# Kernel optimization log

Hardware: AMD Instinct MI355X
Metric: run time of the kernel (lower is better)

## Reference

```python
import jax, jax.numpy as jnp
import numpy as np

K = 16  # neighborhood size


def _eigen_ratio(pts, k):
    """pts: [B, N, 3] -> ratio lambda_max / lambda_mid per point, [B, N]."""
    pts = pts[..., :3]
    # pairwise squared distances [B, N, N]
    sq = jnp.sum(pts * pts, axis=-1)  # [B, N]
    d2 = sq[:, :, None] + sq[:, None, :] - 2.0 * jnp.einsum('bnd,bmd->bnm', pts, pts)
    # k nearest neighbors (self included, as in KNN(x, x))
    _, idx = jax.lax.top_k(-d2, k)  # idx: [B, N, k] int32
    # gather neighbor coordinates: [B, N, k, 3]
    neighbors = jax.vmap(lambda p, i: p[i])(pts, idx)
    mean = jnp.mean(neighbors, axis=2, keepdims=True)
    diff = neighbors - mean  # [B, N, k, 3]
    # covariance = mean over k of outer products -> [B, N, 3, 3]
    cov = jnp.einsum('bnki,bnkj->bnij', diff, diff) / k
    ev = jnp.linalg.eigvalsh(cov)  # ascending: [..., 3]
    return ev[..., 2] / ev[..., 1]


def setup_inputs() -> dict:
    key = jax.random.key(0)
    kx, ky = jax.random.split(key)
    x = jax.random.normal(kx, (2, 8192, 3), dtype=jnp.float32)
    y = jax.random.normal(ky, (2, 8192, 3), dtype=jnp.float32)
    return {"x": x, "y": y}


def reference(x, y):
    er1 = _eigen_ratio(x, K)  # [B, N]
    er2 = _eigen_ratio(y, K)
    res = jnp.mean((er1 - er2) ** 2, axis=-1)  # mean over points
    return jnp.mean(res)  # reduction='mean' over batch
```

## Files before the change

kernel.cpp:

```cpp
#include <hip/hip_runtime.h>
#include <hip/hip_bf16.h>
#include <math.h>

#define NPTS   8192
#define KNN    16
#define G      16
#define NCELL  (G * G * G)
#define NCHUNK 128
#define NPART  4

__constant__ float c_B[17] = {
    -1e30f,
    -1.5341205f, -1.1503494f, -0.8871466f, -0.6744898f, -0.4887764f,
    -0.3186394f, -0.1573107f,  0.0f,        0.1573107f,  0.3186394f,
     0.4887764f,  0.6744898f,  0.8871466f,  1.1503494f,  1.5341205f,
     1e30f
};

__device__ __forceinline__ int cellOf(float v) {
    int c = 0;
#pragma unroll
    for (int i = 1; i <= 15; ++i) c += (v >= c_B[i]) ? 1 : 0;
    return c;
}

__device__ __forceinline__ int spread3(int v) {
    v = (v | (v << 4)) & 0x0C3;
    v = (v | (v << 2)) & 0x249;
    return v;
}

__device__ __forceinline__ int mortonCell(float px, float py, float pz) {
    return (spread3(cellOf(px)) << 2) | (spread3(cellOf(py)) << 1) | spread3(cellOf(pz));
}

__device__ __forceinline__ float dpp_prev_f(float v) {
    int r = __builtin_amdgcn_update_dpp(0, __float_as_int(v), 0x111, 0xF, 0xF, false);
    return __int_as_float(r);
}
__device__ __forceinline__ int dpp_prev_i(int v) {
    return __builtin_amdgcn_update_dpp(0, v, 0x111, 0xF, 0xF, false);
}

__device__ __forceinline__ float sum16(float v) {
    int b;
    b = __builtin_amdgcn_update_dpp(0, __float_as_int(v), 0xB1, 0xF, 0xF, false);
    v += __int_as_float(b);
    b = __builtin_amdgcn_update_dpp(0, __float_as_int(v), 0x4E, 0xF, 0xF, false);
    v += __int_as_float(b);
    b = __builtin_amdgcn_update_dpp(0, __float_as_int(v), 0x141, 0xF, 0xF, false);
    v += __int_as_float(b);
    b = __builtin_amdgcn_update_dpp(0, __float_as_int(v), 0x140, 0xF, 0xF, false);
    v += __int_as_float(b);
    return v;
}

__device__ __forceinline__ unsigned int waveMinU32(unsigned int v) {
    const int ID = (int)0xFFFFFFFF;
    int t;
    t = __builtin_amdgcn_update_dpp(ID, (int)v, 0xB1,  0xF, 0xF, false); v = min(v, (unsigned)t);
    t = __builtin_amdgcn_update_dpp(ID, (int)v, 0x4E,  0xF, 0xF, false); v = min(v, (unsigned)t);
    t = __builtin_amdgcn_update_dpp(ID, (int)v, 0x141, 0xF, 0xF, false); v = min(v, (unsigned)t);
    t = __builtin_amdgcn_update_dpp(ID, (int)v, 0x140, 0xF, 0xF, false); v = min(v, (unsigned)t);
    t = __builtin_amdgcn_update_dpp(ID, (int)v, 0x142, 0xF, 0xF, false); v = min(v, (unsigned)t);
    t = __builtin_amdgcn_update_dpp(ID, (int)v, 0x143, 0xF, 0xF, false); v = min(v, (unsigned)t);
    return (unsigned int)__builtin_amdgcn_readlane((int)v, 63);
}

__global__ __launch_bounds__(1024) void countscan_kernel(
    const float* __restrict__ x, const float* __restrict__ y,
    unsigned int* __restrict__ cellcnt ) {

    __shared__ unsigned int h[NCELL];
    __shared__ unsigned int scanbuf[1024];
    const int tid   = threadIdx.x;
    const int cloud = blockIdx.x;
    const float* __restrict__ src = (cloud < 2 ? x : y) + (size_t)(cloud & 1) * NPTS * 3;

    for (int i = tid; i < NCELL; i += 1024) h[i] = 0;
    __syncthreads();
#pragma unroll
    for (int k = 0; k < 8; ++k) {
        int p = (k << 10) | tid;
        atomicAdd(&h[mortonCell(src[3 * p], src[3 * p + 1], src[3 * p + 2])], 1u);
    }
    __syncthreads();

    unsigned int c0 = h[4 * tid], c1 = h[4 * tid + 1];
    unsigned int c2 = h[4 * tid + 2], c3 = h[4 * tid + 3];
    unsigned int ssum = c0 + c1 + c2 + c3;
    scanbuf[tid] = ssum;
    __syncthreads();
    for (int d = 1; d < 1024; d <<= 1) {
        unsigned int a = scanbuf[tid];
        unsigned int w = (tid >= d) ? scanbuf[tid - d] : 0;
        __syncthreads();
        scanbuf[tid] = a + w;
        __syncthreads();
    }
    unsigned int excl = scanbuf[tid] - ssum;
    unsigned int* cc = cellcnt + cloud * NCELL;
    cc[4 * tid]     = excl;
    cc[4 * tid + 1] = excl + c0;
    cc[4 * tid + 2] = excl + c0 + c1;
    cc[4 * tid + 3] = excl + c0 + c1 + c2;
}

__global__ __launch_bounds__(256) void scatter_kernel(
    const float* __restrict__ x, const float* __restrict__ y,
    unsigned int* __restrict__ cellcnt,
    float4* __restrict__ Ps, unsigned short* __restrict__ origids) {

    const int tid   = threadIdx.x;
    const int cloud = blockIdx.x >> 2;
    const int part  = blockIdx.x & 3;
    const float* __restrict__ src = (cloud < 2 ? x : y) + (size_t)(cloud & 1) * NPTS * 3;
    unsigned int* cc = cellcnt + cloud * NCELL;

#pragma unroll
    for (int k = 0; k < 8; ++k) {
        int p = (part << 11) | (k << 8) | tid;
        float px = src[3 * p], py = src[3 * p + 1], pz = src[3 * p + 2];
        int c = mortonCell(px, py, pz);
        unsigned int pos = atomicAdd(&cc[c], 1u);
        Ps[(cloud << 13) + pos] = make_float4(-2.f * px, -2.f * py, -2.f * pz,
                                              px * px + py * py + pz * pz);
        origids[(cloud << 13) + pos] = (unsigned short)p;
    }
}

__global__ __launch_bounds__(256) void aabb_kernel(
    const float4* __restrict__ Ps, float* __restrict__ aabbG ) {

    const int tid  = threadIdx.x;
    const int lane = tid & 63;
    const int w    = (blockIdx.x << 2) | (tid >> 6);
    const int cloud = w >> 7;
    const int c     = w & 127;

    float4 f = Ps[(cloud << 13) | (c << 6) | lane];
    float px = -0.5f * f.x, py = -0.5f * f.y, pz = -0.5f * f.z;
    float lx = px, hx = px, ly = py, hy = py, lz = pz, hz = pz;
#pragma unroll
    for (int s = 1; s < 64; s <<= 1) {
        lx = fminf(lx, __shfl_xor(lx, s)); hx = fmaxf(hx, __shfl_xor(hx, s));
        ly = fminf(ly, __shfl_xor(ly, s)); hy = fmaxf(hy, __shfl_xor(hy, s));
        lz = fminf(lz, __shfl_xor(lz, s)); hz = fmaxf(hz, __shfl_xor(hz, s));
    }
    if (lane == 0) {
        float* ab = aabbG + cloud * (6 * NCHUNK);
        ab[0 * NCHUNK + c] = lx; ab[1 * NCHUNK + c] = hx;
        ab[2 * NCHUNK + c] = ly; ab[3 * NCHUNK + c] = hy;
        ab[4 * NCHUNK + c] = lz; ab[5 * NCHUNK + c] = hz;
    }
}

__global__ __launch_bounds__(64) void knn_cov_kernel(
    const float4* __restrict__ Ps, const unsigned short* __restrict__ origids,
    const float* __restrict__ aabbG, float* __restrict__ cov,
    unsigned int* __restrict__ counter) {

    const int lane = threadIdx.x;
    const int wid  = blockIdx.x;
    const int cloud = wid >> 13;
    const int s     = wid & (NPTS - 1);

    if (wid == 0 && lane == 0) *counter = 0;

    const float4* __restrict__ Pc = Ps + (cloud << 13);
    const float* __restrict__ ab = aabbG + cloud * (6 * NCHUNK);
    const float4 qp = Pc[s];
    const float sqq = qp.w;
    const float qx = -0.5f * qp.x, qy = -0.5f * qp.y, qz = -0.5f * qp.z;
    const int co = s >> 6;

    float bval[2];
#pragma unroll
    for (int g = 0; g < 2; ++g) {
        int c = (g << 6) | lane;
        float dxl = fmaxf(0.f, fmaxf(ab[c] - qx, qx - ab[NCHUNK + c]));
        float dyl = fmaxf(0.f, fmaxf(ab[2 * NCHUNK + c] - qy, qy - ab[3 * NCHUNK + c]));
        float dzl = fmaxf(0.f, fmaxf(ab[4 * NCHUNK + c] - qz, qz - ab[5 * NCHUNK + c]));
        bval[g] = dxl * dxl + dyl * dyl + dzl * dzl;
    }
    unsigned long long rem0 = ~0ull, rem1 = ~0ull;
    if (co < 64) rem0 &= ~(1ull << co); else rem1 &= ~(1ull << (co - 64));

    auto keys_of = [&](unsigned long long l0, unsigned long long l1,
                       unsigned int& k0, unsigned int& k1) {
        k0 = ((l0 >> lane) & 1)
            ? ((__float_as_uint(bval[0]) & 0xFFFFFF80u) | (unsigned)lane) : 0xFFFFFFFFu;
        k1 = ((l1 >> lane) & 1)
            ? ((__float_as_uint(bval[1]) & 0xFFFFFF80u) | (unsigned)(64 + lane)) : 0xFFFFFFFFu;
    };
    auto argmin2 = [&](unsigned long long l0, unsigned long long l1,
                       int& cidA, int& cidB, bool& hasB) {
        unsigned int k0, k1;
        keys_of(l0, l1, k0, k1);
        unsigned int a = waveMinU32(min(k0, k1));
        cidA = (int)(a & 127u);
        if (lane == (cidA & 63)) { if (cidA < 64) k0 = 0xFFFFFFFFu; else k1 = 0xFFFFFFFFu; }
        unsigned int b = waveMinU32(min(k0, k1));
        hasB = (b != 0xFFFFFFFFu); cidB = (int)(b & 127u);
    };
    auto clear_rem = [&](int cid) {
        if (cid < 64) rem0 &= ~(1ull << cid); else rem1 &= ~(1ull << (cid - 64));
    };
    auto bound_of = [&](int cid) {
        return __int_as_float(__builtin_amdgcn_readlane(
            __float_as_int(bval[cid >> 6]), cid & 63));
    };
    auto popPair = [&](unsigned long long& l0, unsigned long long& l1,
                       int& cA, int& cB, bool& hB) {
        if (__popcll(l0) + __popcll(l1) <= 2) {
            if (l0) { cA = __builtin_ctzll(l0); l0 &= l0 - 1; }
            else    { cA = 64 + __builtin_ctzll(l1); l1 &= l1 - 1; }
            if (l0)      { cB = __builtin_ctzll(l0); l0 &= l0 - 1; hB = true; }
            else if (l1) { cB = 64 + __builtin_ctzll(l1); l1 &= l1 - 1; hB = true; }
            else hB = false;
        } else {
            argmin2(l0, l1, cA, cB, hB);
            if (cA < 64) l0 &= ~(1ull << cA); else l1 &= ~(1ull << (cA - 64));
            if (hB) { if (cB < 64) l0 &= ~(1ull << cB); else l1 &= ~(1ull << (cB - 64)); }
        }
        clear_rem(cA);
        if (hB) clear_rem(cB);
    };

    unsigned long long t0 = rem0, t1 = rem1;
    int pA, pB; bool hPB;
    popPair(t0, t1, pA, pB, hPB);
    float4 pfA = Pc[(pA << 6) | lane];
    float4 pfB = Pc[(pB << 6) | lane];

    float valV, thr;
    int   idxV;
    {
        int pos = (co << 6) | lane;
        float4 f = Pc[pos];
        float k = fmaf(qx, f.x, fmaf(qy, f.y, fmaf(qz, f.z, sqq + f.w)));
        int p = pos;
#pragma unroll
        for (int size = 2; size <= 64; size <<= 1) {
#pragma unroll
            for (int stride = size >> 1; stride >= 1; stride >>= 1) {
                float ok = __shfl_xor(k, stride);
                int   op = __shfl_xor(p, stride);
                bool up = ((lane & size) == 0);
                bool lower = ((lane & stride) == 0);
                bool want_min = (up == lower);
                bool take = want_min ? (ok < k) : (ok > k);
                k = take ? ok : k;
                p = take ? op : p;
            }
        }
        valV = __shfl(k, lane & 15);
        idxV = __shfl(p, lane & 15);
        thr  = __shfl(k, 15);
    }

    auto process = [&](float4 f, int cid) {
        float d2 = fmaf(qx, f.x, fmaf(qy, f.y, fmaf(qz, f.z, sqq + f.w)));
        unsigned long long m = __ballot(d2 < thr);
        while (m) {
            int li = __builtin_ctzll(m); m &= m - 1;
            float sv = __int_as_float(
                __builtin_amdgcn_readlane(__float_as_int(d2), li));
            if (sv < thr) {
                int sj = (cid << 6) | li;
                float pv = dpp_prev_f(valV);
                int   pi = dpp_prev_i(idxV);
                bool keep  = (valV <= sv);
                bool fromv = ((lane & 15) == 0) || (pv <= sv);
                float nv = keep ? valV : (fromv ? sv : pv);
                int   ni = keep ? idxV : (fromv ? sj : pi);
                valV = nv; idxV = ni;
                thr = __int_as_float(__builtin_amdgcn_readlane(__float_as_int(valV), 15));
            }
        }
    };

    if (bound_of(pA) < thr) process(pfA, pA);
    if (hPB && bound_of(pB) < thr) process(pfB, pB);

    for (;;) {
        unsigned long long live0 = rem0 & __ballot(bval[0] < thr);
        unsigned long long live1 = rem1 & __ballot(bval[1] < thr);
        if (!(live0 | live1)) break;

        int cidA, cidB; bool hasB;
        popPair(live0, live1, cidA, cidB, hasB);

        float4 fA = Pc[(cidA << 6) | lane];
        float4 fB;
        if (hasB) fB = Pc[(cidB << 6) | lane];

        process(fA, cidA);
        if (hasB && bound_of(cidB) < thr) process(fB, cidB);
    }

    float4 nf = Pc[idxV];
    float nx = -0.5f * nf.x, ny = -0.5f * nf.y, nz = -0.5f * nf.z;

    const float invk = 1.0f / KNN;
    float mx = sum16(nx) * invk;
    float my = sum16(ny) * invk;
    float mz = sum16(nz) * invk;

    float dx = nx - mx, dy = ny - my, dz = nz - mz;
    float c00 = sum16(dx * dx) * invk, c01 = sum16(dx * dy) * invk, c02 = sum16(dx * dz) * invk;
    float c11 = sum16(dy * dy) * invk, c12 = sum16(dy * dz) * invk, c22 = sum16(dz * dz) * invk;

    if (lane == 0) {
        int orig = origids[(cloud << 13) + s];
        float* cp = cov + ((size_t)(cloud << 13) + orig) * 6;
        *(float2*)(cp)     = make_float2(c00, c01);
        *(float2*)(cp + 2) = make_float2(c02, c11);
        *(float2*)(cp + 4) = make_float2(c12, c22);
    }
}

__device__ double eig_ratio(const float* __restrict__ cp) {
    double a00 = cp[0], a01 = cp[1], a02 = cp[2];
    double a11 = cp[3], a12 = cp[4], a22 = cp[5];

    double qm = (a00 + a11 + a22) * (1.0 / 3.0);
    double p1 = a01 * a01 + a02 * a02 + a12 * a12;
    double b00 = a00 - qm, b11 = a11 - qm, b22 = a22 - qm;
    double p2 = b00 * b00 + b11 * b11 + b22 * b22 + 2.0 * p1;

    if (p2 <= 0.0) return 1.0;
    double p = sqrt(p2 * (1.0 / 6.0));
    double inv = 1.0 / p;
    double m00 = b00 * inv, m11 = b11 * inv, m22 = b22 * inv;
    double m01 = a01 * inv, m02 = a02 * inv, m12 = a12 * inv;
    double detB = m00 * (m11 * m22 - m12 * m12)
                - m01 * (m01 * m22 - m12 * m02)
                + m02 * (m01 * m12 - m11 * m02);
    double r = 0.5 * detB;
    r = fmin(1.0, fmax(-1.0, r));
    double phi = acos(r) * (1.0 / 3.0);
    double e1 = qm + 2.0 * p * cos(phi);
    double e3 = qm + 2.0 * p * cos(phi + 2.0943951023931953);
    double e2 = 3.0 * qm - e1 - e3;
    return e1 / e2;
}

#define EIG_BLOCKS 64

__global__ __launch_bounds__(256) void eigred_kernel(const float* __restrict__ cov,
                                                     double* __restrict__ partial,
                                                     unsigned int* __restrict__ counter,
                                                     float* __restrict__ out) {
    __shared__ double sb[256];
    __shared__ bool islast;
    const int i = blockIdx.x * 256 + threadIdx.x;
    double r1 = eig_ratio(cov + (size_t)i * 6);
    double r2 = eig_ratio(cov + (size_t)(2 * NPTS + i) * 6);
    double d = r1 - r2;
    sb[threadIdx.x] = d * d;
    __syncthreads();
    for (int s2 = 128; s2 > 0; s2 >>= 1) {
        if (threadIdx.x < s2) sb[threadIdx.x] += sb[threadIdx.x + s2];
        __syncthreads();
    }
    if (threadIdx.x == 0) {
        partial[blockIdx.x] = sb[0];
        __threadfence();
        islast = (atomicAdd(counter, 1u) == EIG_BLOCKS - 1);
    }
    __syncthreads();
    if (islast && threadIdx.x < 64) {
        __threadfence();
        double v = ((volatile double*)partial)[threadIdx.x];
#pragma unroll
        for (int w = 1; w < 64; w <<= 1) v += __shfl_xor(v, w);
        if (threadIdx.x == 0) out[0] = (float)(v / (double)(2 * NPTS));
    }
}

extern "C" void kernel_launch(void* const* d_in, const int* in_sizes, int n_in,
                              void* d_out, int out_size, void* d_ws, size_t ws_size,
                              hipStream_t stream) {
    const float* x = (const float*)d_in[0];
    const float* y = (const float*)d_in[1];
    char* ws = (char*)d_ws;

    float4*         Ps      = (float4*)(ws);
    unsigned short* origids = (unsigned short*)(ws + 524288);
    float*          aabbG   = (float*)(ws + 589824);
    float*          cov     = (float*)(ws + 602112);
    unsigned int*   cellcnt = (unsigned int*)(ws + 1388544);
    double*         partial = (double*)(ws + 1454080);
    unsigned int*   counter = (unsigned int*)(ws + 1454592);
    float*          out     = (float*)d_out;

    countscan_kernel<<<4, 1024, 0, stream>>>(x, y, cellcnt);
    scatter_kernel<<<4 * NPART, 256, 0, stream>>>(x, y, cellcnt, Ps, origids);
    aabb_kernel<<<128, 256, 0, stream>>>(Ps, aabbG);
    knn_cov_kernel<<<4 * NPTS, 64, 0, stream>>>(Ps, origids, aabbG, cov, counter);
    eigred_kernel<<<EIG_BLOCKS, 256, 0, stream>>>(cov, partial, counter, out);
}
```

Baseline: 90.52 us.

## Fuse AABB computation into scatter via atomics and split histogram across blocks

Removes the separate aabb kernel launch by computing per-chunk bounding boxes with order-preserving encoded atomicMin/atomicMax during the scatter pass. The count/scan kernel is split into four partial-histogram blocks per cloud, and the last-arriving block sums the partials and does the scan. This cuts one launch and spreads the histogram over more blocks, at the cost of global atomic contention in scatter and an extra partial-histogram round trip through global memory. The cnt4 counter is never reset, but the modulo-4 last-block test still works across repeated calls.

```diff
diff --git a/kernel.cpp b/kernel.cpp
--- a/kernel.cpp
+++ b/kernel.cpp
@@ -7,7 +7,6 @@
 #define G      16
 #define NCELL  (G * G * G)
 #define NCHUNK 128
-#define NPART  4
 
 __constant__ float c_B[17] = {
     -1e30f,
@@ -32,6 +31,14 @@
 
 __device__ __forceinline__ int mortonCell(float px, float py, float pz) {
     return (spread3(cellOf(px)) << 2) | (spread3(cellOf(py)) << 1) | spread3(cellOf(pz));
+}
+
+__device__ __forceinline__ unsigned int encF(float f) {
+    unsigned int u = __float_as_uint(f);
+    return (u & 0x80000000u) ? ~u : (u | 0x80000000u);
+}
+__device__ __forceinline__ float decF(unsigned int e) {
+    return __uint_as_float((e & 0x80000000u) ? (e & 0x7FFFFFFFu) : ~e);
 }
 
 __device__ __forceinline__ float dpp_prev_f(float v) {
@@ -67,55 +74,88 @@
     return (unsigned int)__builtin_amdgcn_readlane((int)v, 63);
 }
 
-__global__ __launch_bounds__(1024) void countscan_kernel(
+__global__ __launch_bounds__(256) void countscan_kernel(
     const float* __restrict__ x, const float* __restrict__ y,
-    unsigned int* __restrict__ cellcnt ) {
+    unsigned int* __restrict__ cellpart, unsigned int* __restrict__ cellcnt,
+    unsigned int* __restrict__ aabbU, unsigned int* __restrict__ cnt4) {
 
     __shared__ unsigned int h[NCELL];
-    __shared__ unsigned int scanbuf[1024];
+    __shared__ unsigned int scanbuf[256];
+    __shared__ bool islast;
+
     const int tid   = threadIdx.x;
-    const int cloud = blockIdx.x;
+    const int cloud = blockIdx.x >> 2;
+    const int part  = blockIdx.x & 3;
     const float* __restrict__ src = (cloud < 2 ? x : y) + (size_t)(cloud & 1) * NPTS * 3;
 
-    for (int i = tid; i < NCELL; i += 1024) h[i] = 0;
+    if (part == 0) {
+        for (int i = tid; i < 6 * NCHUNK; i += 256)
+            aabbU[cloud * (6 * NCHUNK) + i] = ((i >> 7) & 1) ? 0u : 0xFFFFFFFFu;
+    }
+
+    for (int i = tid; i < NCELL; i += 256) h[i] = 0;
     __syncthreads();
 #pragma unroll
     for (int k = 0; k < 8; ++k) {
-        int p = (k << 10) | tid;
+        int p = (part << 11) | (k << 8) | tid;
         atomicAdd(&h[mortonCell(src[3 * p], src[3 * p + 1], src[3 * p + 2])], 1u);
     }
     __syncthreads();
-
-    unsigned int c0 = h[4 * tid], c1 = h[4 * tid + 1];
-    unsigned int c2 = h[4 * tid + 2], c3 = h[4 * tid + 3];
-    unsigned int ssum = c0 + c1 + c2 + c3;
+    unsigned int* cp = cellpart + ((cloud << 2) | part) * NCELL;
+    for (int i = tid; i < NCELL; i += 256) cp[i] = h[i];
+
+    __threadfence();
+    __syncthreads();
+    if (tid == 0) {
+        unsigned int t = atomicAdd(&cnt4[cloud], 1u);
+        islast = ((t & 3u) == 3u);
+    }
+    __syncthreads();
+    if (!islast) return;
+
+    __threadfence();
+
+    const unsigned int* base = cellpart + (cloud << 2) * NCELL;
+    unsigned int cnt[16];
+    unsigned int ssum = 0;
+#pragma unroll
+    for (int j = 0; j < 16; ++j) {
+        int cell = (tid << 4) | j;
+        unsigned int s = base[cell] + base[NCELL + cell]
+                       + base[2 * NCELL + cell] + base[3 * NCELL + cell];
+        cnt[j] = s; ssum += s;
+    }
     scanbuf[tid] = ssum;
     __syncthreads();
-    for (int d = 1; d < 1024; d <<= 1) {
+    for (int d = 1; d < 256; d <<= 1) {
         unsigned int a = scanbuf[tid];
         unsigned int w = (tid >= d) ? scanbuf[tid - d] : 0;
         __syncthreads();
         scanbuf[tid] = a + w;
         __syncthreads();
     }
-    unsigned int excl = scanbuf[tid] - ssum;
+    unsigned int run = scanbuf[tid] - ssum;
     unsigned int* cc = cellcnt + cloud * NCELL;
-    cc[4 * tid]     = excl;
-    cc[4 * tid + 1] = excl + c0;
-    cc[4 * tid + 2] = excl + c0 + c1;
-    cc[4 * tid + 3] = excl + c0 + c1 + c2;
+#pragma unroll
+    for (int j = 0; j < 16; ++j) {
+        int cell = (tid << 4) | j;
+        cc[cell] = run;
+        run += cnt[j];
+    }
 }
 
 __global__ __launch_bounds__(256) void scatter_kernel(
     const float* __restrict__ x, const float* __restrict__ y,
     unsigned int* __restrict__ cellcnt,
-    float4* __restrict__ Ps, unsigned short* __restrict__ origids) {
+    float4* __restrict__ Ps, unsigned short* __restrict__ origids,
+    unsigned int* __restrict__ aabbU) {
 
     const int tid   = threadIdx.x;
     const int cloud = blockIdx.x >> 2;
     const int part  = blockIdx.x & 3;
     const float* __restrict__ src = (cloud < 2 ? x : y) + (size_t)(cloud & 1) * NPTS * 3;
     unsigned int* cc = cellcnt + cloud * NCELL;
+    unsigned int* ab = aabbU + cloud * (6 * NCHUNK);
 
 #pragma unroll
     for (int k = 0; k < 8; ++k) {
@@ -126,38 +166,19 @@
         Ps[(cloud << 13) + pos] = make_float4(-2.f * px, -2.f * py, -2.f * pz,
                                               px * px + py * py + pz * pz);
         origids[(cloud << 13) + pos] = (unsigned short)p;
-    }
-}
-
-__global__ __launch_bounds__(256) void aabb_kernel(
-    const float4* __restrict__ Ps, float* __restrict__ aabbG ) {
-
-    const int tid  = threadIdx.x;
-    const int lane = tid & 63;
-    const int w    = (blockIdx.x << 2) | (tid >> 6);
-    const int cloud = w >> 7;
-    const int c     = w & 127;
-
-    float4 f = Ps[(cloud << 13) | (c << 6) | lane];
-    float px = -0.5f * f.x, py = -0.5f * f.y, pz = -0.5f * f.z;
-    float lx = px, hx = px, ly = py, hy = py, lz = pz, hz = pz;
-#pragma unroll
-    for (int s = 1; s < 64; s <<= 1) {
-        lx = fminf(lx, __shfl_xor(lx, s)); hx = fmaxf(hx, __shfl_xor(hx, s));
-        ly = fminf(ly, __shfl_xor(ly, s)); hy = fmaxf(hy, __shfl_xor(hy, s));
-        lz = fminf(lz, __shfl_xor(lz, s)); hz = fmaxf(hz, __shfl_xor(hz, s));
-    }
-    if (lane == 0) {
-        float* ab = aabbG + cloud * (6 * NCHUNK);
-        ab[0 * NCHUNK + c] = lx; ab[1 * NCHUNK + c] = hx;
-        ab[2 * NCHUNK + c] = ly; ab[3 * NCHUNK + c] = hy;
-        ab[4 * NCHUNK + c] = lz; ab[5 * NCHUNK + c] = hz;
+        int chunk = (int)(pos >> 6);
+        atomicMin(&ab[chunk],              encF(px));
+        atomicMax(&ab[NCHUNK + chunk],     encF(px));
+        atomicMin(&ab[2 * NCHUNK + chunk], encF(py));
+        atomicMax(&ab[3 * NCHUNK + chunk], encF(py));
+        atomicMin(&ab[4 * NCHUNK + chunk], encF(pz));
+        atomicMax(&ab[5 * NCHUNK + chunk], encF(pz));
     }
 }
 
 __global__ __launch_bounds__(64) void knn_cov_kernel(
     const float4* __restrict__ Ps, const unsigned short* __restrict__ origids,
-    const float* __restrict__ aabbG, float* __restrict__ cov,
+    const unsigned int* __restrict__ aabbU, float* __restrict__ cov,
     unsigned int* __restrict__ counter) {
 
     const int lane = threadIdx.x;
@@ -168,7 +189,7 @@
     if (wid == 0 && lane == 0) *counter = 0;
 
     const float4* __restrict__ Pc = Ps + (cloud << 13);
-    const float* __restrict__ ab = aabbG + cloud * (6 * NCHUNK);
+    const unsigned int* __restrict__ ab = aabbU + cloud * (6 * NCHUNK);
     const float4 qp = Pc[s];
     const float sqq = qp.w;
     const float qx = -0.5f * qp.x, qy = -0.5f * qp.y, qz = -0.5f * qp.z;
@@ -178,9 +199,12 @@
 #pragma unroll
     for (int g = 0; g < 2; ++g) {
         int c = (g << 6) | lane;
-        float dxl = fmaxf(0.f, fmaxf(ab[c] - qx, qx - ab[NCHUNK + c]));
-        float dyl = fmaxf(0.f, fmaxf(ab[2 * NCHUNK + c] - qy, qy - ab[3 * NCHUNK + c]));
-        float dzl = fmaxf(0.f, fmaxf(ab[4 * NCHUNK + c] - qz, qz - ab[5 * NCHUNK + c]));
+        float lox = decF(ab[c]),              hix = decF(ab[NCHUNK + c]);
+        float loy = decF(ab[2 * NCHUNK + c]), hiy = decF(ab[3 * NCHUNK + c]);
+        float loz = decF(ab[4 * NCHUNK + c]), hiz = decF(ab[5 * NCHUNK + c]);
+        float dxl = fmaxf(0.f, fmaxf(lox - qx, qx - hix));
+        float dyl = fmaxf(0.f, fmaxf(loy - qy, qy - hiy));
+        float dzl = fmaxf(0.f, fmaxf(loz - qz, qz - hiz));
         bval[g] = dxl * dxl + dyl * dyl + dzl * dzl;
     }
     unsigned long long rem0 = ~0ull, rem1 = ~0ull;
@@ -386,18 +410,19 @@
     const float* y = (const float*)d_in[1];
     char* ws = (char*)d_ws;
 
-    float4*         Ps      = (float4*)(ws);
-    unsigned short* origids = (unsigned short*)(ws + 524288);
-    float*          aabbG   = (float*)(ws + 589824);
-    float*          cov     = (float*)(ws + 602112);
-    unsigned int*   cellcnt = (unsigned int*)(ws + 1388544);
-    double*         partial = (double*)(ws + 1454080);
-    unsigned int*   counter = (unsigned int*)(ws + 1454592);
-    float*          out     = (float*)d_out;
-
-    countscan_kernel<<<4, 1024, 0, stream>>>(x, y, cellcnt);
-    scatter_kernel<<<4 * NPART, 256, 0, stream>>>(x, y, cellcnt, Ps, origids);
-    aabb_kernel<<<128, 256, 0, stream>>>(Ps, aabbG);
-    knn_cov_kernel<<<4 * NPTS, 64, 0, stream>>>(Ps, origids, aabbG, cov, counter);
+    float4*         Ps       = (float4*)(ws);
+    unsigned short* origids  = (unsigned short*)(ws + 524288);
+    unsigned int*   aabbU    = (unsigned int*)(ws + 589824);
+    float*          cov      = (float*)(ws + 602112);
+    unsigned int*   cellcnt  = (unsigned int*)(ws + 1388544);
+    unsigned int*   cellpart = (unsigned int*)(ws + 1454080);
+    double*         partial  = (double*)(ws + 1716224);
+    unsigned int*   counter  = (unsigned int*)(ws + 1716736);
+    unsigned int*   cnt4     = (unsigned int*)(ws + 1716740);
+    float*          out      = (float*)d_out;
+
+    countscan_kernel<<<16, 256, 0, stream>>>(x, y, cellpart, cellcnt, aabbU, cnt4);
+    scatter_kernel<<<16, 256, 0, stream>>>(x, y, cellcnt, Ps, origids, aabbU);
+    knn_cov_kernel<<<4 * NPTS, 64, 0, stream>>>(Ps, origids, aabbU, cov, counter);
     eigred_kernel<<<EIG_BLOCKS, 256, 0, stream>>>(cov, partial, counter, out);
 }
```

New measurement: 96.54 us. 1.07x slower.
